# Optimization experiments

Measured on AMD Instinct MI355X. Metric: run time of the kernel, lower is better.

Reference implementation:

```python
import jax, jax.numpy as jnp
import numpy as np

N_QUBITS = 8
DIM = 2 ** N_QUBITS  # 256


def _apply_1q(state, U, q):
    """Apply a single-qubit gate U on wire q. state: (B, 256) complex64.
    U: (2,2) shared gate or (B,2,2) per-sample gate."""
    B = state.shape[0]
    s = state.reshape(B, 2 ** q, 2, 2 ** (N_QUBITS - 1 - q))
    if U.ndim == 2:
        s = jnp.einsum('ij,bajc->baic', U, s)
    else:
        s = jnp.einsum('bij,bajc->baic', U, s)
    return s.reshape(B, DIM)


def _apply_cnot(state, c, t):
    """CNOT with control wire c, target wire t (pure permutation of amplitudes)."""
    B = state.shape[0]
    a, b = (c, t) if c < t else (t, c)
    s = state.reshape(B, 2 ** a, 2, 2 ** (b - a - 1), 2, 2 ** (N_QUBITS - 1 - b))
    if c < t:
        s0 = s[:, :, 0]                       # control=0: unchanged
        s1 = jnp.flip(s[:, :, 1], axis=3)     # control=1: flip target axis
        s = jnp.stack([s0, s1], axis=2)
    else:
        s0 = s[:, :, :, :, 0]
        s1 = jnp.flip(s[:, :, :, :, 1], axis=2)
        s = jnp.stack([s0, s1], axis=4)
    return s.reshape(B, DIM)


def _rx_batch(theta):
    """Batched RX(theta): (B,) -> (B,2,2) complex64."""
    c = jnp.cos(theta / 2).astype(jnp.complex64)
    s = (-1j * jnp.sin(theta / 2)).astype(jnp.complex64)
    return jnp.stack([jnp.stack([c, s], -1), jnp.stack([s, c], -1)], -2)


def _rot(phi, theta, omega):
    """PennyLane Rot(phi,theta,omega) = RZ(omega) RY(theta) RZ(phi) as a 2x2 matrix."""
    c = jnp.cos(theta / 2)
    s = jnp.sin(theta / 2)
    m00 = jnp.exp(-0.5j * (phi + omega)) * c
    m01 = -jnp.exp(0.5j * (phi - omega)) * s
    m10 = jnp.exp(-0.5j * (phi - omega)) * s
    m11 = jnp.exp(0.5j * (phi + omega)) * c
    return jnp.stack([jnp.stack([m00, m01]), jnp.stack([m10, m11])]).astype(jnp.complex64)


def _circuit(x, weights):
    """AngleEmbedding (RX) + StronglyEntanglingLayers, return <Z_i> per wire: (B,8)."""
    B = x.shape[0]
    state = jnp.zeros((B, DIM), jnp.complex64).at[:, 0].set(1.0)
    # AngleEmbedding: RX(x[:, q]) on wire q
    for q in range(N_QUBITS):
        state = _apply_1q(state, _rx_batch(x[:, q]), q)
    n_layers = weights.shape[0]
    for l in range(n_layers):
        for q in range(N_QUBITS):
            state = _apply_1q(state, _rot(weights[l, q, 0], weights[l, q, 1], weights[l, q, 2]), q)
        r = (l % (N_QUBITS - 1)) + 1  # PennyLane default ranges
        for q in range(N_QUBITS):
            state = _apply_cnot(state, q, (q + r) % N_QUBITS)
    probs = state.real ** 2 + state.imag ** 2  # (B, 256)
    bits = (jnp.arange(DIM)[:, None] >> jnp.arange(N_QUBITS - 1, -1, -1)[None, :]) & 1
    signs = (1.0 - 2.0 * bits).astype(probs.dtype)  # (256, 8); wire 0 = MSB
    return probs @ signs  # (B, 8) expectation values of PauliZ


def setup_inputs() -> dict:
    key = jax.random.key(0)
    k1, k2, k3 = jax.random.split(key, 3)
    B = 32768
    x = jax.random.uniform(k1, (B, N_QUBITS), dtype=jnp.float32)
    weights = jax.random.uniform(k2, (2, N_QUBITS, 3), dtype=jnp.float32, maxval=2.0 * np.pi)
    fc_w = jax.random.normal(k3, (1, N_QUBITS), dtype=jnp.float32) / np.sqrt(N_QUBITS)
    fc_b = jnp.zeros((1,), jnp.float32)
    return {"x": x, "weights": weights, "fc_w": fc_w, "fc_b": fc_b}


def reference(x, weights, fc_w, fc_b):
    z = _circuit(x, weights)                 # (B, 8)
    return jax.nn.sigmoid(z @ fc_w.T + fc_b)  # (B, 1)
```

## Files before the change

### kernel.cpp

```cpp
#include <hip/hip_runtime.h>
#include <hip/hip_fp16.h>
#include <math.h>

#define NQ 8

__host__ __device__ constexpr int cnot_step(int i, int c, int t) {
    return ((i >> (7 - c)) & 1) ? (i ^ (1 << (7 - t))) : i;
}
__host__ __device__ constexpr int sigma_fwd(int i, int r) {
    for (int q = 0; q < 8; ++q) i = cnot_step(i, q, (q + r) & 7);
    return i;
}
__host__ __device__ constexpr int sigma_inv(int i, int r) {
    for (int q = 7; q >= 0; --q) i = cnot_step(i, q, (q + r) & 7);
    return i;
}
__host__ __device__ constexpr int pairmask(int q) { return sigma_inv(1 << (7 - q), 1); }
__host__ __device__ constexpr int rolemask(int q) {
    int m = 0;
    for (int j = 0; j < 8; ++j)
        if ((sigma_fwd(1 << j, 1) >> (7 - q)) & 1) m |= 1 << j;
    return m;
}
__host__ __device__ constexpr int colmask2(int b) {
    return sigma_fwd(sigma_fwd(1 << b, 1), 2);
}

__host__ __device__ constexpr int amp_index(int slot, int k, int hl) {
    return (slot << 7) | (((k >> 3) & 1) << 6) | ((hl & 1) << 5) | (((hl >> 1) & 1) << 4)
         | (((hl >> 2) & 1) << 3) | (((k >> 2) & 1) << 2) | (((k >> 1) & 1) << 1) | (k & 1);
}
__host__ __device__ constexpr int mask_slot(int M) { return (M >> 7) & 1; }
__host__ __device__ constexpr int mask_k(int M) {
    return (((M >> 6) & 1) << 3) | (((M >> 2) & 1) << 2) | (((M >> 1) & 1) << 1) | (M & 1);
}
__host__ __device__ constexpr int mask_l(int M) {
    return ((M >> 5) & 1) | (((M >> 4) & 1) << 1) | (((M >> 3) & 1) << 2);
}

typedef _Float16 h2v __attribute__((ext_vector_type(2)));

__device__ __forceinline__ __half2 bc_h2(uint32_t u) { return __builtin_bit_cast(__half2, u); }
__device__ __forceinline__ uint32_t bc_u32(__half2 h) { return __builtin_bit_cast(uint32_t, h); }
__device__ __forceinline__ h2v bc_hv(__half2 h) { return __builtin_bit_cast(h2v, h); }
__device__ __forceinline__ uint32_t rot16(uint32_t u) { return (u >> 16) | (u << 16); }

template<int XM>
__device__ __forceinline__ uint32_t swzu(uint32_t v) {
    return (uint32_t)__builtin_amdgcn_ds_swizzle((int)v, (XM << 10) | 0x1F);
}
template<int CTRL>
__device__ __forceinline__ uint32_t dppx(uint32_t v) {
    return (uint32_t)__builtin_amdgcn_update_dpp(0, (int)v, CTRL, 0xF, 0xF, true);
}
template<int CTRL>
__device__ __forceinline__ float dppaddf(float v) {
    const uint32_t p = (uint32_t)__builtin_amdgcn_update_dpp(
        0, (int)__builtin_bit_cast(uint32_t, v), CTRL, 0xF, 0xF, true);
    return v + __builtin_bit_cast(float, p);
}

__device__ __forceinline__ void cmul(float& zr, float& zi,
                                     float xr, float xi, float yr, float yi) {
    const float tr = xr * yr - xi * yi;
    const float ti = xr * yi + xi * yr;
    zr = tr; zi = ti;
}

struct H2C { __half2 re, im; };
struct YB  { __half2 re, im, imn; };
__device__ __forceinline__ YB mkyb(float r, float i) {
    YB y;
    y.re  = __floats2half2_rn(r, r);
    y.im  = __floats2half2_rn(i, i);
    y.imn = bc_h2(bc_u32(y.im) ^ 0x80008000u);
    return y;
}
__device__ __forceinline__ H2C h2c_mul(H2C x, YB y) {
    H2C z;
    z.re = __hfma2(x.im, y.imn, __hmul2(x.re, y.re));
    z.im = __hfma2(x.im, y.re,  __hmul2(x.re, y.im));
    return z;
}

template<int Q>
__device__ __forceinline__ void gateQ(__half2 re[16], __half2 im[16], int hl,
                                      const uint32_t* __restrict__ cw)
{
    constexpr int M  = pairmask(Q);
    constexpr int RM = rolemask(Q);
    constexpr int mk = mask_k(M);
    constexpr int ml = mask_l(M);
    constexpr int ms = mask_slot(M);
    constexpr int rk = mask_k(RM);
    constexpr int rl = mask_l(RM);

    const uint4    c4v = *(const uint4*)(cw + Q * 8);
    const uint32_t WDn = cw[Q * 8 + 4];

    const uint32_t pm = (uint32_t)(__popc(hl & rl) & 1) * 0x80008000u;
    const uint32_t Bp = c4v.y ^ pm, Bn = Bp ^ 0x80008000u;
    const uint32_t Cp = c4v.z ^ pm, Cn = Cp ^ 0x80008000u;
    const __half2  Aw = bc_h2(c4v.x);
    const __half2  Dw = bc_h2(c4v.w);
    const __half2  Dn = bc_h2(WDn);

    auto prep = [](uint32_t v) -> uint32_t {
        if constexpr (ms) v = rot16(v);
        if constexpr (ml == 1) v = dppx<0xB1>(v);
        else if constexpr (ml == 3) v = dppx<0x1B>(v);
        else if constexpr (ml != 0) v = swzu<ml>(v);
        return v;
    };
    auto upd = [&](int k, uint32_t pr, uint32_t pi) {
        const bool par = (__popc(k & rk) & 1) != 0;
        const __half2 B1 = bc_h2(par ? Bn : Bp);
        const __half2 B2 = bc_h2(par ? Bp : Bn);
        const __half2 Cc = bc_h2(par ? Cn : Cp);
        __half2 nr = __hmul2(Aw, re[k]);
        nr = __hfma2(B1, im[k], nr);
        nr = __hfma2(Cc, bc_h2(pr), nr);
        nr = __hfma2(Dw, bc_h2(pi), nr);
        __half2 ni = __hmul2(Aw, im[k]);
        ni = __hfma2(B2, re[k], ni);
        ni = __hfma2(Cc, bc_h2(pi), ni);
        ni = __hfma2(Dn, bc_h2(pr), ni);
        re[k] = nr; im[k] = ni;
    };

    if constexpr (mk == 0) {
#pragma unroll
        for (int k = 0; k < 16; ++k) {
            const uint32_t pr = prep(bc_u32(re[k]));
            const uint32_t pi = prep(bc_u32(im[k]));
            upd(k, pr, pi);
        }
    } else {
        constexpr int msb = (mk & 8) ? 8 : ((mk & 4) ? 4 : ((mk & 2) ? 2 : 1));
#pragma unroll
        for (int k = 0; k < 16; ++k) {
            if ((k & msb) != 0) continue;
            const int k2 = k ^ mk;
            const uint32_t pr_k  = prep(bc_u32(re[k2]));
            const uint32_t pi_k  = prep(bc_u32(im[k2]));
            const uint32_t pr_k2 = prep(bc_u32(re[k]));
            const uint32_t pi_k2 = prep(bc_u32(im[k]));
            upd(k,  pr_k,  pi_k);
            upd(k2, pr_k2, pi_k2);
        }
    }
}

__global__ __launch_bounds__(256) void vqe_fused(
    const float* __restrict__ x,
    const float* __restrict__ weights,
    const float* __restrict__ fc_w,
    const float* __restrict__ fc_b,
    float* __restrict__ out, int B)
{
    __shared__ __align__(16) float    g0[64];
    __shared__ __align__(16) uint32_t cw[64];
    __shared__ __align__(16) float    cols[32 * 36];
    __shared__ __align__(16) uint32_t wth2[8 * 20];

    const int t = threadIdx.x;

    if (t < 8) {
        const float* w3 = weights + t * 3;
        float s, c;   __sincosf(w3[1] * 0.5f, &s, &c);
        float sa, ca; __sincosf(0.5f * (w3[0] + w3[2]), &sa, &ca);
        float sb, cb; __sincosf(0.5f * (w3[0] - w3[2]), &sb, &cb);
        float* g = g0 + t * 8;
        g[0] = c * ca;  g[1] = -c * sa;
        g[2] = -s * cb; g[3] = -s * sb;
        g[4] = s * cb;  g[5] = -s * sb;
        g[6] = c * ca;  g[7] = c * sa;
    } else if (t < 16) {
        const int q = t - 8;
        const float* w3 = weights + (NQ + q) * 3;
        float s, c;   __sincosf(w3[1] * 0.5f, &s, &c);
        float sa, ca; __sincosf(0.5f * (w3[0] + w3[2]), &sa, &ca);
        float sb, cb; __sincosf(0.5f * (w3[0] - w3[2]), &sb, &cb);
        const float A = c * ca, Bc = c * sa, C = s * cb, D = s * sb;
        const float s1 = (rolemask(q) & 0x80) ? -1.f : 1.f;
        uint32_t* cq = cw + q * 8;
        cq[0] = bc_u32(__floats2half2_rn(A, A));
        cq[1] = bc_u32(__floats2half2_rn(Bc, s1 * Bc));
        cq[2] = bc_u32(__floats2half2_rn(-C, -s1 * C));
        cq[3] = bc_u32(__floats2half2_rn(D, D));
        cq[4] = bc_u32(__floats2half2_rn(-D, -D));
        cq[5] = 0; cq[6] = 0; cq[7] = 0;
    } else if (t >= 128) {
        const int tt = t - 128;
        const int whl = tt >> 4, wk = tt & 15;
        float wsl[2];
#pragma unroll
        for (int slot = 0; slot < 2; ++slot) {
            const int s = amp_index(slot, wk, whl);
            int j = 0;
#pragma unroll
            for (int b = 0; b < 8; ++b)
                if ((s >> b) & 1) j ^= colmask2(b);
            float w = 0.f;
#pragma unroll
            for (int q = 0; q < 8; ++q)
                w += ((j >> (7 - q)) & 1) ? -fc_w[q] : fc_w[q];
            wsl[slot] = w;
        }
        wth2[whl * 20 + wk] = bc_u32(__floats2half2_rn(wsl[0], wsl[1]));
    }
    __syncthreads();

    {
        const int s = t >> 3, q = t & 7;
        const int sg = blockIdx.x * 32 + s;
        if (sg < B) {
            const float xv = x[sg * NQ + q];
            float sn, cs; __sincosf(xv * 0.5f, &sn, &cs);
            const float* g = g0 + q * 8;
            float* c = cols + s * 36 + q * 4;
            c[0] = cs * g[0] + sn * g[3];
            c[1] = cs * g[1] - sn * g[2];
            c[2] = cs * g[4] + sn * g[7];
            c[3] = cs * g[5] - sn * g[6];
        }
    }
    __syncthreads();

    const int lane = t & 63;
    const int hl   = lane & 7;
    const int sidx = ((t >> 6) << 3) | ((lane >> 3) & 7);
    const int samp = blockIdx.x * 32 + sidx;
    if (samp >= B) return;

    const float* cb = cols + sidx * 36;

    const float2 e2 = *(const float2*)(cb + 2 * 4 + (hl & 1) * 2);
    const float2 e3 = *(const float2*)(cb + 3 * 4 + ((hl >> 1) & 1) * 2);
    const float2 e4 = *(const float2*)(cb + 4 * 4 + ((hl >> 2) & 1) * 2);
    float cr = e2.x, ci = e2.y;
    cmul(cr, ci, cr, ci, e3.x, e3.y);
    cmul(cr, ci, cr, ci, e4.x, e4.y);

    const float4 c0 = *(const float4*)(cb + 0 * 4);
    const float4 c1 = *(const float4*)(cb + 1 * 4);
    const float4 c5 = *(const float4*)(cb + 5 * 4);
    const float4 c6 = *(const float4*)(cb + 6 * 4);
    const float4 c7 = *(const float4*)(cb + 7 * 4);

    float w0r, w0i, w1r, w1i;
    cmul(w0r, w0i, cr, ci, c0.x, c0.y);
    cmul(w1r, w1i, cr, ci, c0.z, c0.w);
    H2C S{__floats2half2_rn(w0r, w1r), __floats2half2_rn(w0i, w1i)};

    const YB y1a = mkyb(c1.x, c1.y), y1b = mkyb(c1.z, c1.w);
    const YB y5a = mkyb(c5.x, c5.y), y5b = mkyb(c5.z, c5.w);
    const YB y6a = mkyb(c6.x, c6.y), y6b = mkyb(c6.z, c6.w);
    const YB y7a = mkyb(c7.x, c7.y), y7b = mkyb(c7.z, c7.w);

    const H2C A0 = h2c_mul(S, y1a);
    const H2C A1 = h2c_mul(S, y1b);
    H2C Bv[4];
    Bv[0] = h2c_mul(A0, y5a); Bv[1] = h2c_mul(A0, y5b);
    Bv[2] = h2c_mul(A1, y5a); Bv[3] = h2c_mul(A1, y5b);
    H2C Cv[8];
#pragma unroll
    for (int j = 0; j < 4; ++j) {
        Cv[j * 2 + 0] = h2c_mul(Bv[j], y6a);
        Cv[j * 2 + 1] = h2c_mul(Bv[j], y6b);
    }
    __half2 re[16], im[16];
#pragma unroll
    for (int j = 0; j < 8; ++j) {
        const H2C z0 = h2c_mul(Cv[j], y7a);
        const H2C z1 = h2c_mul(Cv[j], y7b);
        re[j * 2 + 0] = z0.re; im[j * 2 + 0] = z0.im;
        re[j * 2 + 1] = z1.re; im[j * 2 + 1] = z1.im;
    }

    gateQ<0>(re, im, hl, cw);
    gateQ<1>(re, im, hl, cw);
    gateQ<2>(re, im, hl, cw);
    gateQ<3>(re, im, hl, cw);
    gateQ<4>(re, im, hl, cw);
    gateQ<5>(re, im, hl, cw);
    gateQ<6>(re, im, hl, cw);
    gateQ<7>(re, im, hl, cw);

    const uint32_t* wrow = wth2 + hl * 20;
    const uint4 wa = *(const uint4*)(wrow + 0);
    const uint4 wb = *(const uint4*)(wrow + 4);
    const uint4 wc = *(const uint4*)(wrow + 8);
    const uint4 wd = *(const uint4*)(wrow + 12);
    const uint32_t wkw[16] = {wa.x, wa.y, wa.z, wa.w, wb.x, wb.y, wb.z, wb.w,
                              wc.x, wc.y, wc.z, wc.w, wd.x, wd.y, wd.z, wd.w};

    float acc = 0.f;
#pragma unroll
    for (int k = 0; k < 16; ++k) {
        const __half2 W = bc_h2(wkw[k]);
        const __half2 tr_ = __hmul2(re[k], W);
        const __half2 ti_ = __hmul2(im[k], W);
#if defined(__has_builtin) && __has_builtin(__builtin_amdgcn_fdot2)
        acc = __builtin_amdgcn_fdot2(bc_hv(tr_), bc_hv(re[k]), acc, false);
        acc = __builtin_amdgcn_fdot2(bc_hv(ti_), bc_hv(im[k]), acc, false);
#else
        acc += __low2float(tr_) * __low2float(re[k]) + __high2float(tr_) * __high2float(re[k]);
        acc += __low2float(ti_) * __low2float(im[k]) + __high2float(ti_) * __high2float(im[k]);
#endif
    }
    acc = dppaddf<0xB1>(acc);
    acc = dppaddf<0x4E>(acc);
    acc = dppaddf<0x141>(acc);

    if (hl == 0) {
        const float z = acc + fc_b[0];
        out[samp] = 1.0f / (1.0f + __expf(-z));
    }
}

extern "C" void kernel_launch(void* const* d_in, const int* in_sizes, int n_in,
                              void* d_out, int out_size, void* d_ws, size_t ws_size,
                              hipStream_t stream) {
    const float* x       = (const float*)d_in[0];
    const float* weights = (const float*)d_in[1];
    const float* fc_w    = (const float*)d_in[2];
    const float* fc_b    = (const float*)d_in[3];
    float* out = (float*)d_out;
    (void)d_ws; (void)ws_size;

    const int B = in_sizes[0] / NQ;
    const int blocks = (B + 31) / 32;

    vqe_fused<<<blocks, 256, 0, stream>>>(x, weights, fc_w, fc_b, out, B);
}
```

Baseline: 18.20 us.

## Split each sample's state across 16 lanes instead of 8

Each sample's 256 amplitudes now live across 16 lanes holding 8 half2 registers each, where before 8 lanes held 16 each. The lane-to-bit mapping of the index is redone to match, which adds a DPP 0x4E path and a swizzle step to the final reduction. Blocks now cover 16 samples, so twice as many blocks launch. The aim is lower register pressure and more thread parallelism per sample, at the cost of more cross-lane shuffles per gate and extra per-block setup.

Result: slower. 19.12 us (+5.0%).

```diff
diff --git a/kernel.cpp b/kernel.cpp
--- a/kernel.cpp
+++ b/kernel.cpp
@@ -27,15 +27,15 @@
 }
 
 __host__ __device__ constexpr int amp_index(int slot, int k, int hl) {
-    return (slot << 7) | (((k >> 3) & 1) << 6) | ((hl & 1) << 5) | (((hl >> 1) & 1) << 4)
-         | (((hl >> 2) & 1) << 3) | (((k >> 2) & 1) << 2) | (((k >> 1) & 1) << 1) | (k & 1);
+    return (slot << 7) | (((k >> 2) & 1) << 6) | ((hl & 1) << 5) | (((hl >> 2) & 1) << 4)
+         | (((hl >> 3) & 1) << 3) | (((hl >> 1) & 1) << 2) | (((k >> 1) & 1) << 1) | (k & 1);
 }
 __host__ __device__ constexpr int mask_slot(int M) { return (M >> 7) & 1; }
 __host__ __device__ constexpr int mask_k(int M) {
-    return (((M >> 6) & 1) << 3) | (((M >> 2) & 1) << 2) | (((M >> 1) & 1) << 1) | (M & 1);
+    return (((M >> 6) & 1) << 2) | (((M >> 1) & 1) << 1) | (M & 1);
 }
 __host__ __device__ constexpr int mask_l(int M) {
-    return ((M >> 5) & 1) | (((M >> 4) & 1) << 1) | (((M >> 3) & 1) << 2);
+    return ((M >> 5) & 1) * 1 + (((M >> 4) & 1)) * 4 + (((M >> 3) & 1)) * 8 + (((M >> 2) & 1)) * 2;
 }
 
 typedef _Float16 h2v __attribute__((ext_vector_type(2)));
@@ -48,6 +48,11 @@
 template<int XM>
 __device__ __forceinline__ uint32_t swzu(uint32_t v) {
     return (uint32_t)__builtin_amdgcn_ds_swizzle((int)v, (XM << 10) | 0x1F);
+}
+template<int XM>
+__device__ __forceinline__ float swzf(float v) {
+    return __builtin_bit_cast(float, (uint32_t)__builtin_amdgcn_ds_swizzle(
+        (int)__builtin_bit_cast(uint32_t, v), (XM << 10) | 0x1F));
 }
 template<int CTRL>
 __device__ __forceinline__ uint32_t dppx(uint32_t v) {
@@ -84,7 +89,7 @@
 }
 
 template<int Q>
-__device__ __forceinline__ void gateQ(__half2 re[16], __half2 im[16], int hl,
+__device__ __forceinline__ void gateQ(__half2 re[8], __half2 im[8], int hl,
                                       const uint32_t* __restrict__ cw)
 {
     constexpr int M  = pairmask(Q);
@@ -108,6 +113,7 @@
     auto prep = [](uint32_t v) -> uint32_t {
         if constexpr (ms) v = rot16(v);
         if constexpr (ml == 1) v = dppx<0xB1>(v);
+        else if constexpr (ml == 2) v = dppx<0x4E>(v);
         else if constexpr (ml == 3) v = dppx<0x1B>(v);
         else if constexpr (ml != 0) v = swzu<ml>(v);
         return v;
@@ -130,15 +136,15 @@
 
     if constexpr (mk == 0) {
 #pragma unroll
-        for (int k = 0; k < 16; ++k) {
+        for (int k = 0; k < 8; ++k) {
             const uint32_t pr = prep(bc_u32(re[k]));
             const uint32_t pi = prep(bc_u32(im[k]));
             upd(k, pr, pi);
         }
     } else {
-        constexpr int msb = (mk & 8) ? 8 : ((mk & 4) ? 4 : ((mk & 2) ? 2 : 1));
-#pragma unroll
-        for (int k = 0; k < 16; ++k) {
+        constexpr int msb = (mk & 4) ? 4 : ((mk & 2) ? 2 : 1);
+#pragma unroll
+        for (int k = 0; k < 8; ++k) {
             if ((k & msb) != 0) continue;
             const int k2 = k ^ mk;
             const uint32_t pr_k  = prep(bc_u32(re[k2]));
@@ -160,8 +166,8 @@
 {
     __shared__ __align__(16) float    g0[64];
     __shared__ __align__(16) uint32_t cw[64];
-    __shared__ __align__(16) float    cols[32 * 36];
-    __shared__ __align__(16) uint32_t wth2[8 * 20];
+    __shared__ __align__(16) float    cols[16 * 36];
+    __shared__ __align__(16) uint32_t wth2[16 * 12];
 
     const int t = threadIdx.x;
 
@@ -192,7 +198,7 @@
         cq[5] = 0; cq[6] = 0; cq[7] = 0;
     } else if (t >= 128) {
         const int tt = t - 128;
-        const int whl = tt >> 4, wk = tt & 15;
+        const int whl = tt >> 3, wk = tt & 7;
         float wsl[2];
 #pragma unroll
         for (int slot = 0; slot < 2; ++slot) {
@@ -207,13 +213,13 @@
                 w += ((j >> (7 - q)) & 1) ? -fc_w[q] : fc_w[q];
             wsl[slot] = w;
         }
-        wth2[whl * 20 + wk] = bc_u32(__floats2half2_rn(wsl[0], wsl[1]));
+        wth2[whl * 12 + wk] = bc_u32(__floats2half2_rn(wsl[0], wsl[1]));
     }
     __syncthreads();
 
-    {
+    if (t < 128) {
         const int s = t >> 3, q = t & 7;
-        const int sg = blockIdx.x * 32 + s;
+        const int sg = blockIdx.x * 16 + s;
         if (sg < B) {
             const float xv = x[sg * NQ + q];
             float sn, cs; __sincosf(xv * 0.5f, &sn, &cs);
@@ -228,23 +234,24 @@
     __syncthreads();
 
     const int lane = t & 63;
-    const int hl   = lane & 7;
-    const int sidx = ((t >> 6) << 3) | ((lane >> 3) & 7);
-    const int samp = blockIdx.x * 32 + sidx;
+    const int hl   = lane & 15;
+    const int sidx = ((t >> 6) << 2) | ((lane >> 4) & 3);
+    const int samp = blockIdx.x * 16 + sidx;
     if (samp >= B) return;
 
     const float* cb = cols + sidx * 36;
 
     const float2 e2 = *(const float2*)(cb + 2 * 4 + (hl & 1) * 2);
-    const float2 e3 = *(const float2*)(cb + 3 * 4 + ((hl >> 1) & 1) * 2);
-    const float2 e4 = *(const float2*)(cb + 4 * 4 + ((hl >> 2) & 1) * 2);
+    const float2 e3 = *(const float2*)(cb + 3 * 4 + ((hl >> 2) & 1) * 2);
+    const float2 e4 = *(const float2*)(cb + 4 * 4 + ((hl >> 3) & 1) * 2);
+    const float2 e5 = *(const float2*)(cb + 5 * 4 + ((hl >> 1) & 1) * 2);
     float cr = e2.x, ci = e2.y;
     cmul(cr, ci, cr, ci, e3.x, e3.y);
     cmul(cr, ci, cr, ci, e4.x, e4.y);
+    cmul(cr, ci, cr, ci, e5.x, e5.y);
 
     const float4 c0 = *(const float4*)(cb + 0 * 4);
     const float4 c1 = *(const float4*)(cb + 1 * 4);
-    const float4 c5 = *(const float4*)(cb + 5 * 4);
     const float4 c6 = *(const float4*)(cb + 6 * 4);
     const float4 c7 = *(const float4*)(cb + 7 * 4);
 
@@ -254,26 +261,19 @@
     H2C S{__floats2half2_rn(w0r, w1r), __floats2half2_rn(w0i, w1i)};
 
     const YB y1a = mkyb(c1.x, c1.y), y1b = mkyb(c1.z, c1.w);
-    const YB y5a = mkyb(c5.x, c5.y), y5b = mkyb(c5.z, c5.w);
     const YB y6a = mkyb(c6.x, c6.y), y6b = mkyb(c6.z, c6.w);
     const YB y7a = mkyb(c7.x, c7.y), y7b = mkyb(c7.z, c7.w);
 
     const H2C A0 = h2c_mul(S, y1a);
     const H2C A1 = h2c_mul(S, y1b);
     H2C Bv[4];
-    Bv[0] = h2c_mul(A0, y5a); Bv[1] = h2c_mul(A0, y5b);
-    Bv[2] = h2c_mul(A1, y5a); Bv[3] = h2c_mul(A1, y5b);
-    H2C Cv[8];
+    Bv[0] = h2c_mul(A0, y6a); Bv[1] = h2c_mul(A0, y6b);
+    Bv[2] = h2c_mul(A1, y6a); Bv[3] = h2c_mul(A1, y6b);
+    __half2 re[8], im[8];
 #pragma unroll
     for (int j = 0; j < 4; ++j) {
-        Cv[j * 2 + 0] = h2c_mul(Bv[j], y6a);
-        Cv[j * 2 + 1] = h2c_mul(Bv[j], y6b);
-    }
-    __half2 re[16], im[16];
-#pragma unroll
-    for (int j = 0; j < 8; ++j) {
-        const H2C z0 = h2c_mul(Cv[j], y7a);
-        const H2C z1 = h2c_mul(Cv[j], y7b);
+        const H2C z0 = h2c_mul(Bv[j], y7a);
+        const H2C z1 = h2c_mul(Bv[j], y7b);
         re[j * 2 + 0] = z0.re; im[j * 2 + 0] = z0.im;
         re[j * 2 + 1] = z1.re; im[j * 2 + 1] = z1.im;
     }
@@ -287,17 +287,14 @@
     gateQ<6>(re, im, hl, cw);
     gateQ<7>(re, im, hl, cw);
 
-    const uint32_t* wrow = wth2 + hl * 20;
+    const uint32_t* wrow = wth2 + hl * 12;
     const uint4 wa = *(const uint4*)(wrow + 0);
     const uint4 wb = *(const uint4*)(wrow + 4);
-    const uint4 wc = *(const uint4*)(wrow + 8);
-    const uint4 wd = *(const uint4*)(wrow + 12);
-    const uint32_t wkw[16] = {wa.x, wa.y, wa.z, wa.w, wb.x, wb.y, wb.z, wb.w,
-                              wc.x, wc.y, wc.z, wc.w, wd.x, wd.y, wd.z, wd.w};
+    const uint32_t wkw[8] = {wa.x, wa.y, wa.z, wa.w, wb.x, wb.y, wb.z, wb.w};
 
     float acc = 0.f;
 #pragma unroll
-    for (int k = 0; k < 16; ++k) {
+    for (int k = 0; k < 8; ++k) {
         const __half2 W = bc_h2(wkw[k]);
         const __half2 tr_ = __hmul2(re[k], W);
         const __half2 ti_ = __hmul2(im[k], W);
@@ -311,7 +308,8 @@
     }
     acc = dppaddf<0xB1>(acc);
     acc = dppaddf<0x4E>(acc);
-    acc = dppaddf<0x141>(acc);
+    acc = dppaddf<0x140>(acc);
+    acc += swzf<4>(acc);
 
     if (hl == 0) {
         const float z = acc + fc_b[0];
@@ -330,7 +328,7 @@
     (void)d_ws; (void)ws_size;
 
     const int B = in_sizes[0] / NQ;
-    const int blocks = (B + 31) / 32;
+    const int blocks = (B + 15) / 16;
 
     vqe_fused<<<blocks, 256, 0, stream>>>(x, weights, fc_w, fc_b, out, B);
 }
```

## Replace block barrier with wave-local wait and prefetch gate coefficients into registers

Applied to the files above, without the earlier changes.

Each wave now computes the column coefficients only for its own samples, so the second block-wide __syncthreads can become a wave-local LDS wait plus a scheduling barrier. All gate coefficients from LDS are loaded once into registers up front and passed into the gate routine, instead of being read inside each gate step. This removes a block barrier and lets the LDS loads overlap with the initial state construction, at the cost of about 40 extra live registers that may reduce occupancy. Correctness depends on the sample-to-wave mapping matching exactly between the producer and consumer phases.

Measured after the change: 18.03 us. About the same (-0.9%).

```diff
diff --git a/kernel.cpp b/kernel.cpp
--- a/kernel.cpp
+++ b/kernel.cpp
@@ -85,7 +85,8 @@
 
 template<int Q>
 __device__ __forceinline__ void gateQ(__half2 re[16], __half2 im[16], int hl,
-                                      const uint32_t* __restrict__ cw)
+                                      uint32_t wAu, uint32_t wBu, uint32_t wCu,
+                                      uint32_t wDu, uint32_t wDnu)
 {
     constexpr int M  = pairmask(Q);
     constexpr int RM = rolemask(Q);
@@ -95,15 +96,12 @@
     constexpr int rk = mask_k(RM);
     constexpr int rl = mask_l(RM);
 
-    const uint4    c4v = *(const uint4*)(cw + Q * 8);
-    const uint32_t WDn = cw[Q * 8 + 4];
-
     const uint32_t pm = (uint32_t)(__popc(hl & rl) & 1) * 0x80008000u;
-    const uint32_t Bp = c4v.y ^ pm, Bn = Bp ^ 0x80008000u;
-    const uint32_t Cp = c4v.z ^ pm, Cn = Cp ^ 0x80008000u;
-    const __half2  Aw = bc_h2(c4v.x);
-    const __half2  Dw = bc_h2(c4v.w);
-    const __half2  Dn = bc_h2(WDn);
+    const uint32_t Bp = wBu ^ pm, Bn = Bp ^ 0x80008000u;
+    const uint32_t Cp = wCu ^ pm, Cn = Cp ^ 0x80008000u;
+    const __half2  Aw = bc_h2(wAu);
+    const __half2  Dw = bc_h2(wDu);
+    const __half2  Dn = bc_h2(wDnu);
 
     auto prep = [](uint32_t v) -> uint32_t {
         if constexpr (ms) v = rot16(v);
@@ -212,7 +210,9 @@
     __syncthreads();
 
     {
-        const int s = t >> 3, q = t & 7;
+        const int lane6 = t & 63;
+        const int s = ((t >> 6) << 3) | (lane6 >> 3);
+        const int q = lane6 & 7;
         const int sg = blockIdx.x * 32 + s;
         if (sg < B) {
             const float xv = x[sg * NQ + q];
@@ -225,7 +225,8 @@
             c[3] = cs * g[5] - sn * g[6];
         }
     }
-    __syncthreads();
+    asm volatile("s_waitcnt lgkmcnt(0)" ::: "memory");
+    __builtin_amdgcn_sched_barrier(0);
 
     const int lane = t & 63;
     const int hl   = lane & 7;
@@ -238,15 +239,26 @@
     const float2 e2 = *(const float2*)(cb + 2 * 4 + (hl & 1) * 2);
     const float2 e3 = *(const float2*)(cb + 3 * 4 + ((hl >> 1) & 1) * 2);
     const float2 e4 = *(const float2*)(cb + 4 * 4 + ((hl >> 2) & 1) * 2);
-    float cr = e2.x, ci = e2.y;
-    cmul(cr, ci, cr, ci, e3.x, e3.y);
-    cmul(cr, ci, cr, ci, e4.x, e4.y);
-
     const float4 c0 = *(const float4*)(cb + 0 * 4);
     const float4 c1 = *(const float4*)(cb + 1 * 4);
     const float4 c5 = *(const float4*)(cb + 5 * 4);
     const float4 c6 = *(const float4*)(cb + 6 * 4);
     const float4 c7 = *(const float4*)(cb + 7 * 4);
+
+    uint32_t cc[40];
+#pragma unroll
+    for (int qg = 0; qg < 8; ++qg) {
+        const uint4 v4 = *(const uint4*)(cw + qg * 8);
+        cc[qg * 5 + 0] = v4.x;
+        cc[qg * 5 + 1] = v4.y;
+        cc[qg * 5 + 2] = v4.z;
+        cc[qg * 5 + 3] = v4.w;
+        cc[qg * 5 + 4] = cw[qg * 8 + 4];
+    }
+
+    float cr = e2.x, ci = e2.y;
+    cmul(cr, ci, cr, ci, e3.x, e3.y);
+    cmul(cr, ci, cr, ci, e4.x, e4.y);
 
     float w0r, w0i, w1r, w1i;
     cmul(w0r, w0i, cr, ci, c0.x, c0.y);
@@ -278,14 +290,14 @@
         re[j * 2 + 1] = z1.re; im[j * 2 + 1] = z1.im;
     }
 
-    gateQ<0>(re, im, hl, cw);
-    gateQ<1>(re, im, hl, cw);
-    gateQ<2>(re, im, hl, cw);
-    gateQ<3>(re, im, hl, cw);
-    gateQ<4>(re, im, hl, cw);
-    gateQ<5>(re, im, hl, cw);
-    gateQ<6>(re, im, hl, cw);
-    gateQ<7>(re, im, hl, cw);
+    gateQ<0>(re, im, hl, cc[ 0], cc[ 1], cc[ 2], cc[ 3], cc[ 4]);
+    gateQ<1>(re, im, hl, cc[ 5], cc[ 6], cc[ 7], cc[ 8], cc[ 9]);
+    gateQ<2>(re, im, hl, cc[10], cc[11], cc[12], cc[13], cc[14]);
+    gateQ<3>(re, im, hl, cc[15], cc[16], cc[17], cc[18], cc[19]);
+    gateQ<4>(re, im, hl, cc[20], cc[21], cc[22], cc[23], cc[24]);
+    gateQ<5>(re, im, hl, cc[25], cc[26], cc[27], cc[28], cc[29]);
+    gateQ<6>(re, im, hl, cc[30], cc[31], cc[32], cc[33], cc[34]);
+    gateQ<7>(re, im, hl, cc[35], cc[36], cc[37], cc[38], cc[39]);
 
     const uint32_t* wrow = wth2 + hl * 20;
     const uint4 wa = *(const uint4*)(wrow + 0);
```
